# Performance work log

Measured on AMD Instinct MI355X. Metric: run time of the kernel, lower is better.

## Reference

```python
import jax, jax.numpy as jnp
from jax import lax
import numpy as np

EPS = 2.220446049250313e-16  # sys.float_info.epsilon


def setup_inputs() -> dict:
    key = jax.random.key(0)
    k1, k2, k3, k4 = jax.random.split(key, 4)
    C, H, W, R = 256, 256, 256, 16
    x = jax.random.normal(k1, (1, C, H, W), dtype=jnp.float32)
    w1 = jax.random.normal(k2, (R, C), dtype=jnp.float32) * 0.05   # Linear(C -> C//r), no bias
    w2 = jax.random.normal(k3, (C, R), dtype=jnp.float32) * 0.05   # Linear(C//r -> C), no bias
    conv_w = jax.random.normal(k4, (1, 2, 7, 7), dtype=jnp.float32) * 0.05  # Conv2d(2,1,7)
    return {"x": x, "w1": w1, "w2": w2, "conv_w": conv_w, "kv": 1}


def reference(x, w1, w2, conv_w, kv):
    b, c, h, w = x.shape  # b == 1 (module assumes batch 1 via squeeze(0))

    def fc(v):  # shared MLP of the channel attention
        return jnp.maximum(v @ w1.T, 0.0) @ w2.T

    y_avg = fc(x.mean(axis=(2, 3)))          # [1, C]
    y_max = fc(x.max(axis=(2, 3)))           # [1, C]
    y = jax.nn.sigmoid(y_avg + y_max)        # [1, C]

    yc = y[0]
    yc = (yc - yc.min()) / (yc.max() - yc.min() + 1e-20)  # min-max normalized gates in [0,1]

    # Batched SVD over channels replaces the per-channel Python loop.
    mats = x[0]                                            # [C, H, W]
    u, s, vh = jnp.linalg.svd(mats, full_matrices=False)   # u:[C,H,K] s:[C,K] vh:[C,K,W]
    K = s.shape[-1]
    # k = int(len(s) * kv * yc[c]); singular values are sorted descending, so
    # top-k selection == keep the first k -> mask the tail.
    k = jnp.floor(K * kv * yc).astype(jnp.int32)           # [C]
    keep = jnp.arange(K)[None, :] < k[:, None]             # [C, K]
    s_m = jnp.where(keep, s, 0.0)
    recon = jnp.einsum('chk,ck,ckw->chw', u, s_m, vh)      # low-rank reconstruction
    x2 = recon[None]                                       # [1, C, H, W]

    avg_out = x2.mean(axis=1, keepdims=True)
    max_out = x2.max(axis=1, keepdims=True)
    cat = jnp.concatenate([avg_out, max_out], axis=1)      # [1, 2, H, W]
    out = lax.conv_general_dilated(cat, conv_w, (1, 1), [(3, 3), (3, 3)],
                                   dimension_numbers=('NCHW', 'OIHW', 'NCHW'))
    out = jnp.where(out < EPS, EPS, out)
    return jax.nn.sigmoid(out)
```

## Files before the change

### kernel.cpp

```cpp
#include <hip/hip_runtime.h>


#define NCH 256
#define N 256
#define NN 65536
#define NS_MAX 22

#define OFF_K 0
#define OFF_MODE 256
#define OFF_MC 512
#define OFF_COEF 768
#define OFF_SUM 12032
#define OFF_MAXHW 77568
#define OFF_MEAND 143104
#define OFF_MAXD 143616
#define OFF_T 144128
#define OFF_ALPHA 144640
#define OFF_AQ 145152
#define OFF_BQ 276224
#define OFF_ITSW 407296
#define SMALL_FLOATS 407552

#define NSH_LDS 135168
#define F16_PANEL 33792

static const float EPSF = 2.220446049250313e-16f;

typedef unsigned short u16;
typedef _Float16 h8 __attribute__((ext_vector_type(8)));
typedef float f32x4 __attribute__((ext_vector_type(4)));

__device__ __forceinline__ float rdlane(float v, int l) {
  return __uint_as_float(__builtin_amdgcn_readlane(__float_as_uint(v), l));
}

__device__ __forceinline__ u16 f2h(float v) {
  _Float16 h = (_Float16)v;
  u16 u;
  __builtin_memcpy(&u, &h, 2);
  return u;
}
__device__ __forceinline__ float h2f(u16 u) {
  _Float16 h;
  __builtin_memcpy(&h, &u, 2);
  return (float)h;
}

__global__ __launch_bounds__(256) void k_chan_stats(const float* __restrict__ x,
                                                    float* __restrict__ small) {
  int c = blockIdx.x, tid = threadIdx.x;
  const float4* xc = (const float4*)(x + (size_t)c * NN);
  double s = 0.0;
  float m = -1e30f;
  for (int i = tid; i < NN / 4; i += 256) {
    float4 v = xc[i];
    s += (double)v.x + (double)v.y + (double)v.z + (double)v.w;
    m = fmaxf(m, fmaxf(fmaxf(v.x, v.y), fmaxf(v.z, v.w)));
  }
  __shared__ double rs[4];
  __shared__ float rm[4];
  for (int off = 32; off; off >>= 1) {
    s += __shfl_down(s, off, 64);
    m = fmaxf(m, __shfl_down(m, off, 64));
  }
  if ((tid & 63) == 0) { rs[tid >> 6] = s; rm[tid >> 6] = m; }
  __syncthreads();
  if (tid == 0) {
    ((double*)(small + OFF_MEAND))[c] = (rs[0] + rs[1] + rs[2] + rs[3]) / (double)NN;
    ((double*)(small + OFF_MAXD))[c] =
        (double)fmaxf(fmaxf(rm[0], rm[1]), fmaxf(rm[2], rm[3]));
  }
}

__global__ __launch_bounds__(256) void k_attention(const float* __restrict__ w1,
                                                   const float* __restrict__ w2,
                                                   const int* __restrict__ kvp,
                                                   float* __restrict__ small) {
  int tid = threadIdx.x;
  __shared__ double ha[16], hm[16], redd[8], ymn[256], ymx[256];
  double va = ((const double*)(small + OFF_MEAND))[tid];
  double vm = ((const double*)(small + OFF_MAXD))[tid];
  for (int r = 0; r < 16; ++r) {
    double wv = (double)w1[r * 256 + tid];
    double pa = wv * va, pm = wv * vm;
    for (int off = 32; off; off >>= 1) {
      pa += __shfl_down(pa, off, 64);
      pm += __shfl_down(pm, off, 64);
    }
    if ((tid & 63) == 0) { redd[tid >> 6] = pa; redd[4 + (tid >> 6)] = pm; }
    __syncthreads();
    if (tid == 0) {
      ha[r] = fmax(redd[0] + redd[1] + redd[2] + redd[3], 0.0);
      hm[r] = fmax(redd[4] + redd[5] + redd[6] + redd[7], 0.0);
    }
    __syncthreads();
  }
  double ya = 0.0, ym = 0.0;
  for (int r = 0; r < 16; ++r) {
    double wv = (double)w2[tid * 16 + r];
    ya += ha[r] * wv;
    ym += hm[r] * wv;
  }
  double y = 1.0 / (1.0 + exp(-(ya + ym)));
  ymn[tid] = y; ymx[tid] = y;
  __syncthreads();
  for (int off = 128; off; off >>= 1) {
    if (tid < off) {
      ymn[tid] = fmin(ymn[tid], ymn[tid + off]);
      ymx[tid] = fmax(ymx[tid], ymx[tid + off]);
    }
    __syncthreads();
  }
  double yc = (y - ymn[0]) / (ymx[0] - ymn[0] + 1e-20);
  int kv = kvp[0];
  int k = (int)floor(256.0 * (double)kv * yc);
  int mode = (k <= 0) ? 0 : ((k >= 256) ? 1 : 2);
  int* ip = (int*)small;
  ip[OFF_K + tid] = k;
  ip[OFF_MODE + tid] = mode;
}

#define GEMM128_VARS                                                           \
  int tid = threadIdx.x;                                                       \
  int tx4 = (tid & 15) * 4, ty4 = (tid >> 4) * 4;                              \
  int lm = tid >> 1, lq = (tid & 1) * 2;                                       \
  int lk = tid >> 4, lc = (tid & 15) * 2;                                      \
  (void)lk; (void)lc;

#define STORE_T128(Ls, v0, v1)                                                 \
  Ls[lq * 4 + 0][lm] = v0.x; Ls[lq * 4 + 1][lm] = v0.y;                        \
  Ls[lq * 4 + 2][lm] = v0.z; Ls[lq * 4 + 3][lm] = v0.w;                        \
  Ls[lq * 4 + 4][lm] = v1.x; Ls[lq * 4 + 5][lm] = v1.y;                        \
  Ls[lq * 4 + 6][lm] = v1.z; Ls[lq * 4 + 7][lm] = v1.w;

#define GEMM128_INNER(AsM, BsM)                                                \
  _Pragma("unroll") for (int kk = 0; kk < 16; ++kk) {                          \
    float4 a0 = *(const float4*)&AsM[kk][ty4];                                 \
    float4 a1 = *(const float4*)&AsM[kk][64 + ty4];                            \
    float4 b0 = *(const float4*)&BsM[kk][tx4];                                 \
    float4 b1 = *(const float4*)&BsM[kk][64 + tx4];                            \
    float av[8] = {a0.x, a0.y, a0.z, a0.w, a1.x, a1.y, a1.z, a1.w};            \
    float bv[8] = {b0.x, b0.y, b0.z, b0.w, b1.x, b1.y, b1.z, b1.w};            \
    _Pragma("unroll") for (int rr = 0; rr < 8; ++rr)                           \
      _Pragma("unroll") for (int cc2 = 0; cc2 < 8; ++cc2)                      \
        acc[rr][cc2] += av[rr] * bv[cc2];                                      \
  }

#define WRITE_TILE_NORM(Cc)                                                    \
  _Pragma("unroll") for (int rh = 0; rh < 2; ++rh)                             \
  _Pragma("unroll") for (int rr = 0; rr < 4; ++rr) {                           \
    int rI = rh * 4 + rr;                                                      \
    float* rowp = (Cc) + (size_t)(i0 + rh * 64 + ty4 + rr) * N + j0;           \
    *(float4*)(rowp + tx4) =                                                   \
        make_float4(acc[rI][0], acc[rI][1], acc[rI][2], acc[rI][3]);           \
    *(float4*)(rowp + 64 + tx4) =                                              \
        make_float4(acc[rI][4], acc[rI][5], acc[rI][6], acc[rI][7]);           \
  }

#define WRITE_TILE_MIRROR(Cc)                                                  \
  _Pragma("unroll") for (int ch = 0; ch < 2; ++ch)                             \
  _Pragma("unroll") for (int cc2 = 0; cc2 < 4; ++cc2) {                        \
    int cI = ch * 4 + cc2;                                                     \
    float* rowp = (Cc) + (size_t)(j0 + ch * 64 + tx4 + cc2) * N + i0;          \
    *(float4*)(rowp + ty4) =                                                   \
        make_float4(acc[0][cI], acc[1][cI], acc[2][cI], acc[3][cI]);           \
    *(float4*)(rowp + 64 + ty4) =                                              \
        make_float4(acc[4][cI], acc[5][cI], acc[6][cI], acc[7][cI]);           \
  }

#define SYM_MAP                                                                \
  int bx = blockIdx.x;                                                         \
  int i0 = (bx >= 1) ? 128 : 0, j0 = (bx == 2) ? 128 : 0;

__global__ __launch_bounds__(256) void k_gram(const float* __restrict__ x,
                                              float* __restrict__ bufA, int base) {
  __shared__ float As[16][132], Bs[16][132];
  GEMM128_VARS; SYM_MAP;
  const float* A = x + (size_t)(base + blockIdx.z) * NN;
  float acc[8][8] = {};
  const float* Ap = A + (size_t)(i0 + lm) * N + lq * 4;
  const float* Bp = A + (size_t)(j0 + lm) * N + lq * 4;
  float4 va0 = *(const float4*)Ap, va1 = *(const float4*)(Ap + 4);
  float4 vb0 = *(const float4*)Bp, vb1 = *(const float4*)(Bp + 4);
  for (int kt = 0; kt < 16; ++kt) {
    __syncthreads();
    STORE_T128(As, va0, va1); STORE_T128(Bs, vb0, vb1);
    __syncthreads();
    if (kt < 15) {
      va0 = *(const float4*)(Ap + (kt + 1) * 16);
      va1 = *(const float4*)(Ap + (kt + 1) * 16 + 4);
      vb0 = *(const float4*)(Bp + (kt + 1) * 16);
      vb1 = *(const float4*)(Bp + (kt + 1) * 16 + 4);
    }
    GEMM128_INNER(As, Bs);
  }
  float* Cc = bufA + (size_t)blockIdx.z * NN;
  WRITE_TILE_NORM(Cc);
  if (bx == 1) { WRITE_TILE_MIRROR(Cc); }
}

__device__ __forceinline__ double mv_chunk(const float* __restrict__ P, int c0,
                                           int j, int r, int R0, int triR,
                                           float ureg) {
  double pi0 = 0.0, pi1 = 0.0, pi2 = 0.0, pi3 = 0.0;
  if (c0 < N) {
    int lbeg = (c0 > j + 1) ? c0 : (j + 1);
    int lend = c0 + 64;
    if (lbeg < lend) {
      if (c0 + 64 <= R0) {
        int lmv = lbeg;
        for (; lmv + 3 < lend; lmv += 4) {
          float uv0 = rdlane(ureg, lmv - c0), uv1 = rdlane(ureg, lmv + 1 - c0);
          float uv2 = rdlane(ureg, lmv + 2 - c0), uv3 = rdlane(ureg, lmv + 3 - c0);
          float v0 = P[triR + lmv], v1 = P[triR + lmv + 1];
          float v2 = P[triR + lmv + 2], v3 = P[triR + lmv + 3];
          pi0 += (double)v0 * (double)uv0;
          pi1 += (double)v1 * (double)uv1;
          pi2 += (double)v2 * (double)uv2;
          pi3 += (double)v3 * (double)uv3;
        }
        for (; lmv < lend; ++lmv)
          pi0 += (double)P[triR + lmv] * (double)rdlane(ureg, lmv - c0);
      } else if (c0 >= R0 + 64) {
        int lmv = lbeg;
        int s = (lmv * (lmv + 1)) >> 1;
        for (; lmv + 3 < lend; lmv += 4) {
          int s0 = s, s1 = s0 + lmv + 1, s2 = s1 + lmv + 2, s3 = s2 + lmv + 3;
          s = s3 + lmv + 4;
          float uv0 = rdlane(ureg, lmv - c0), uv1 = rdlane(ureg, lmv + 1 - c0);
          float uv2 = rdlane(ureg, lmv + 2 - c0), uv3 = rdlane(ureg, lmv + 3 - c0);
          pi0 += (double)P[s0 + r] * (double)uv0;
          pi1 += (double)P[s1 + r] * (double)uv1;
          pi2 += (double)P[s2 + r] * (double)uv2;
          pi3 += (double)P[s3 + r] * (double)uv3;
        }
        for (; lmv < lend; ++lmv) {
          pi0 += (double)P[s + r] * (double)rdlane(ureg, lmv - c0);
          s += lmv + 1;
        }
      } else {
        int lmv = lbeg;
        int s = (lmv * (lmv + 1)) >> 1;
        for (; lmv < lend; ++lmv) {
          float uv = rdlane(ureg, lmv - c0);
          float v = P[(lmv <= r) ? (triR + lmv) : (s + r)];
          pi0 += (double)v * (double)uv;
          s += lmv + 1;
        }
      }
    }
  }
  return (pi0 + pi1) + (pi2 + pi3);
}

__device__ __forceinline__ void upd_chunk(float* __restrict__ P, int c0, int j,
                                          int r, int R0, int triR, float ureg,
                                          float wreg, float urf, float wrf) {
  if (c0 >= N) return;
  int lbeg = (c0 > j + 1) ? c0 : (j + 1);
  int lend = c0 + 64;
  int lcap = (r | 63) + 1;
  if (lend > lcap) lend = lcap;
  if (c0 + 64 <= R0) {
    int lmv = lbeg;
    for (; lmv + 1 < lend; lmv += 2) {
      float uv0 = rdlane(ureg, lmv - c0), wv0 = rdlane(wreg, lmv - c0);
      float uv1 = rdlane(ureg, lmv + 1 - c0), wv1 = rdlane(wreg, lmv + 1 - c0);
      P[triR + lmv] = fmaf(-wrf, uv0, fmaf(-urf, wv0, P[triR + lmv]));
      P[triR + lmv + 1] = fmaf(-wrf, uv1, fmaf(-urf, wv1, P[triR + lmv + 1]));
    }
    if (lmv < lend) {
      float uv0 = rdlane(ureg, lmv - c0), wv0 = rdlane(wreg, lmv - c0);
      P[triR + lmv] = fmaf(-wrf, uv0, fmaf(-urf, wv0, P[triR + lmv]));
    }
  } else if (c0 == R0) {
    for (int lmv = lbeg; lmv < lend; ++lmv) {
      float uv = rdlane(ureg, lmv - c0), wv = rdlane(wreg, lmv - c0);
      if (lmv <= r)
        P[triR + lmv] = fmaf(-wrf, uv, fmaf(-urf, wv, P[triR + lmv]));
    }
  }
}

__global__ __launch_bounds__(1024) void k_tridiag(const float* __restrict__ Gall,
                                                  float* __restrict__ small, int base) {
  extern __shared__ double dls[];
  double* redd = dls;
  double* redd2 = dls + 16;
  double* pip = dls + 32;
  float* P = (float*)(dls + 1056);
  float* uf = P + 32896;
  float* wf = uf + 256;
  int tid = threadIdx.x, lane = tid & 63;
  int r = tid & 255, g = tid >> 8;
  int wid = tid >> 6;
  int R0 = (wid & 3) << 6;
  int c = base + blockIdx.x;
  const int* ip = (const int*)small;
  if (ip[OFF_MODE + c] != 2) return;
  const float* G = Gall + (size_t)blockIdx.x * NN;
  double* aq = (double*)(small + OFF_AQ) + (size_t)c * 256;
  double* bq = (double*)(small + OFF_BQ) + (size_t)c * 256;
  const int triR = (r * (r + 1)) >> 1;

  for (int i = g; i < N; i += 4)
    if (r <= i) P[((i * (i + 1)) >> 1) + r] = G[i * N + r];
  __syncthreads();

  for (int j = 0; j + 2 < N; ++j) {
    if (g == 0 && r >= j + 1) uf[r] = P[triR + j];
    __syncthreads();
    float x_r = uf[r];
    double x0 = (double)uf[j + 1];
    int cbase = (j + 1) & ~63;
    int c0 = cbase + 64 * g;
    float ureg = 0.f;
    if (c0 < N) ureg = uf[c0 + lane];
    double sp = (g == 0 && r >= j + 2) ? (double)x_r * (double)x_r : 0.0;
    double myp = mv_chunk(P, c0, j, r, R0, triR, ureg);
    pip[tid] = (r >= j + 1) ? myp : 0.0;
    for (int off = 32; off; off >>= 1) sp += __shfl_down(sp, off, 64);
    if (lane == 0) redd[wid] = sp;
    __syncthreads();
    double sigma = (((redd[0] + redd[1]) + (redd[2] + redd[3])) +
                    ((redd[4] + redd[5]) + (redd[6] + redd[7]))) +
                   (((redd[8] + redd[9]) + (redd[10] + redd[11])) +
                    ((redd[12] + redd[13]) + (redd[14] + redd[15])));
    if (sigma <= 1e-40) {
      if (tid == 0) bq[j] = x0;
      continue;
    }
    double nu = sqrt(x0 * x0 + sigma);
    double bsub = (x0 >= 0.0) ? -nu : nu;
    double beta = 1.0 / (nu * (nu + fabs(x0)));
    if (c0 <= j + 1 && j + 1 < c0 + 64 && lane == j + 1 - c0)
      ureg = (float)(x0 - bsub);
    double pi = 0.0, u_r = 0.0, kp = 0.0;
    if (r >= j + 1) {
      double fix = -bsub * (double)P[triR + (j + 1)];
      pi = (pip[r] + pip[256 + r] + pip[512 + r] + pip[768 + r] + fix) * beta;
      u_r = (r == j + 1) ? (x0 - bsub) : (double)x_r;
      kp = u_r * pi * 0.25;
    }
    for (int off = 32; off; off >>= 1) kp += __shfl_down(kp, off, 64);
    if (lane == 0) redd2[wid] = kp;
    __syncthreads();
    double K = ((((redd2[0] + redd2[1]) + (redd2[2] + redd2[3])) +
                 ((redd2[4] + redd2[5]) + (redd2[6] + redd2[7]))) +
                (((redd2[8] + redd2[9]) + (redd2[10] + redd2[11])) +
                 ((redd2[12] + redd2[13]) + (redd2[14] + redd2[15])))) *
               beta * 0.5;
    if (g == 0 && r >= j + 1) wf[r] = (float)(pi - K * u_r);
    __syncthreads();
    float wreg = 0.f;
    if (c0 < N) wreg = wf[c0 + lane];
    if (r >= j + 1) {
      float urf = (float)u_r;
      float wrf = wf[r];
      upd_chunk(P, c0, j, r, R0, triR, ureg, wreg, urf, wrf);
    }
    if (tid == 0) bq[j] = bsub;
    __syncthreads();
  }
  if (g == 0) aq[r] = (double)P[triR + r];
  if (tid == 0) bq[N - 2] = (double)P[(((N - 1) * N) >> 1) + N - 2];
}

__device__ __forceinline__ int sturm_count_lds(const double* a, const double* b,
                                               double t) {
  double d = a[0] - t;
  int cnt = (d < 0.0);
  for (int i = 1; i < N; ++i) {
    double den = d;
    if (fabs(den) < 1e-20) den = (den < 0.0) ? -1e-20 : 1e-20;
    double bb = b[i - 1];
    d = (a[i] - t) - bb * bb / den;
    cnt += (d < 0.0);
  }
  return cnt;
}

__global__ __launch_bounds__(64) void k_bisect(float* __restrict__ small,
                                               int base, int cc) {
  int ci = blockIdx.x;
  if (ci >= cc) return;
  int c = base + ci, lane = threadIdx.x;
  int* ip = (int*)small;
  if (ip[OFF_MODE + c] != 2) {
    if (lane == 0) { ip[OFF_MC + c] = 0; ip[OFF_ITSW + c] = 0; }
    return;
  }
  int k = ip[OFF_K + c];
  const double* a = (const double*)(small + OFF_AQ) + (size_t)c * 256;
  const double* b = (const double*)(small + OFF_BQ) + (size_t)c * 256;
  __shared__ double sa[256], sb[256];
  for (int i = lane; i < N; i += 64) {
    sa[i] = a[i];
    if (i < N - 1) sb[i] = b[i];
  }
  __syncthreads();
  double lo = 1e300, hi = -1e300;
  for (int i = lane; i < N; i += 64) {
    double rr = (i > 0 ? fabs(sb[i - 1]) : 0.0) + (i < N - 1 ? fabs(sb[i]) : 0.0);
    lo = fmin(lo, sa[i] - rr);
    hi = fmax(hi, sa[i] + rr);
  }
  for (int off = 32; off; off >>= 1) {
    lo = fmin(lo, __shfl_xor(lo, off, 64));
    hi = fmax(hi, __shfl_xor(hi, off, 64));
  }
  double lamk = 0.0, lamk1 = 0.0;
  for (int which = 0; which < 2; ++which) {
    int j = (which == 0) ? (N - k + 1) : (N - k);
    double l0 = lo, h0 = hi;
    for (int pass = 0; pass < 10; ++pass) {
      double step = (h0 - l0) * (1.0 / 65.0);
      double t = l0 + step * (double)(lane + 1);
      int cnt = sturm_count_lds(sa, sb, t);
      unsigned long long mask = __ballot(cnt >= j);
      if (mask == 0ull) {
        l0 = l0 + step * 64.0;
      } else {
        int bpos = __ffsll((long long)mask) - 1;
        double nl = (bpos == 0) ? l0 : (l0 + step * (double)bpos);
        h0 = l0 + step * (double)(bpos + 1);
        l0 = nl;
      }
    }
    double v = 0.5 * (l0 + h0);
    if (which == 0) lamk = v; else lamk1 = v;
  }
  if (lane == 0) {
    double t = 0.5 * (lamk + lamk1);
    double gap = fmax(lamk - lamk1, 0.0);
    double alpha = 1.002 * fmax(hi - t, t - lo) + 1e-30;
    double g0 = fmax(gap / (2.0 * alpha), 2e-6);
    float* cf = small + OFF_COEF + (size_t)c * (2 * NS_MAX);
    double l = fmin(g0, 0.99);
    int m = 0, isw = NS_MAX;
    while (m < NS_MAX - 2 && l < 0.9999) {
      if (isw == NS_MAX && l >= 0.02) isw = m;
      double aa = sqrt(27.0 / (4.0 * (1.0 + l + l * l)));
      double bb = (4.0 / 27.0) * aa * aa * aa;
      cf[2 * m] = (float)aa;
      cf[2 * m + 1] = (float)bb;
      double pl = aa * l - bb * l * l * l;
      double p1 = aa - bb;
      l = fmin(pl, p1);
      m++;
    }
    for (int e = 0; e < 2; ++e) {
      if (isw == NS_MAX && l >= 0.02) isw = m;
      cf[2 * m] = 1.5f; cf[2 * m + 1] = 0.5f; m++;
    }
    if (isw > m) isw = m;
    ip[OFF_MC + c] = m;
    ip[OFF_ITSW + c] = isw;
    ((double*)(small + OFF_T))[c] = t;
    ((double*)(small + OFF_ALPHA))[c] = alpha;
  }
}

__global__ void k_x0(const float* __restrict__ small, float* __restrict__ bufA,
                     int base) {
  int ci = blockIdx.y, c = base + ci;
  const int* ip = (const int*)small;
  if (ip[OFF_MODE + c] != 2) return;
  double t = ((const double*)(small + OFF_T))[c];
  double inva = 1.0 / ((const double*)(small + OFF_ALPHA))[c];
  float* X = bufA + (size_t)ci * NN;
  int r = blockIdx.x, tid = threadIdx.x;
  double gg = (double)X[r * N + tid];
  if (tid == r) gg -= t;
  X[r * N + tid] = (float)(gg * inva);
}

__global__ __launch_bounds__(256) void k_ns1(const float* __restrict__ src,
                                             float* __restrict__ Sb,
                                             const float* __restrict__ small,
                                             int base, int it) {
  const int* ip = (const int*)small;
  int c = base + blockIdx.z;
  if (ip[OFF_MODE + c] != 2 || it >= ip[OFF_ITSW + c]) return;
  __shared__ float As[16][132], Bs[16][132];
  GEMM128_VARS; SYM_MAP;
  const float* X = src + (size_t)blockIdx.z * NN;
  float acc[8][8] = {};
  const float* Ap = X + (size_t)(i0 + lm) * N + lq * 4;
  const float* Bp = X + (size_t)(j0 + lm) * N + lq * 4;
  float4 va0 = *(const float4*)Ap, va1 = *(const float4*)(Ap + 4);
  float4 vb0 = *(const float4*)Bp, vb1 = *(const float4*)(Bp + 4);
  for (int kt = 0; kt < 16; ++kt) {
    __syncthreads();
    STORE_T128(As, va0, va1); STORE_T128(Bs, vb0, vb1);
    __syncthreads();
    if (kt < 15) {
      va0 = *(const float4*)(Ap + (kt + 1) * 16);
      va1 = *(const float4*)(Ap + (kt + 1) * 16 + 4);
      vb0 = *(const float4*)(Bp + (kt + 1) * 16);
      vb1 = *(const float4*)(Bp + (kt + 1) * 16 + 4);
    }
    GEMM128_INNER(As, Bs);
  }
  float* Cc = Sb + (size_t)blockIdx.z * NN;
  WRITE_TILE_NORM(Cc);
  if (bx == 1) { WRITE_TILE_MIRROR(Cc); }
}

__global__ __launch_bounds__(256) void k_ns2(const float* __restrict__ src,
                                             const float* __restrict__ Sb,
                                             float* __restrict__ dst,
                                             const float* __restrict__ small,
                                             int base, int it) {
  const int* ip = (const int*)small;
  int c = base + blockIdx.z;
  if (ip[OFF_MODE + c] != 2 || it >= ip[OFF_ITSW + c]) return;
  float ca = small[OFF_COEF + (size_t)c * (2 * NS_MAX) + 2 * it];
  float cb = small[OFF_COEF + (size_t)c * (2 * NS_MAX) + 2 * it + 1];
  __shared__ float As[16][132], Bs[16][132];
  GEMM128_VARS; SYM_MAP;
  const float* X = src + (size_t)blockIdx.z * NN;
  const float* S = Sb + (size_t)blockIdx.z * NN;
  float acc[8][8] = {};
  const float* Ap = X + (size_t)(i0 + lm) * N + lq * 4;
  const float* Bp = S + (size_t)(j0 + lm) * N + lq * 4;
  float4 va0 = *(const float4*)Ap, va1 = *(const float4*)(Ap + 4);
  float4 vb0 = *(const float4*)Bp, vb1 = *(const float4*)(Bp + 4);
  for (int kt = 0; kt < 16; ++kt) {
    __syncthreads();
    STORE_T128(As, va0, va1); STORE_T128(Bs, vb0, vb1);
    __syncthreads();
    if (kt < 15) {
      va0 = *(const float4*)(Ap + (kt + 1) * 16);
      va1 = *(const float4*)(Ap + (kt + 1) * 16 + 4);
      vb0 = *(const float4*)(Bp + (kt + 1) * 16);
      vb1 = *(const float4*)(Bp + (kt + 1) * 16 + 4);
    }
    GEMM128_INNER(As, Bs);
  }
#pragma unroll
  for (int rh = 0; rh < 2; ++rh)
#pragma unroll
    for (int rr = 0; rr < 4; ++rr) {
      int rI = rh * 4 + rr;
      const float* rowp = X + (size_t)(i0 + rh * 64 + ty4 + rr) * N + j0;
      float4 x0 = *(const float4*)(rowp + tx4);
      float4 x1 = *(const float4*)(rowp + 64 + tx4);
      acc[rI][0] = ca * x0.x - cb * acc[rI][0];
      acc[rI][1] = ca * x0.y - cb * acc[rI][1];
      acc[rI][2] = ca * x0.z - cb * acc[rI][2];
      acc[rI][3] = ca * x0.w - cb * acc[rI][3];
      acc[rI][4] = ca * x1.x - cb * acc[rI][4];
      acc[rI][5] = ca * x1.y - cb * acc[rI][5];
      acc[rI][6] = ca * x1.z - cb * acc[rI][6];
      acc[rI][7] = ca * x1.w - cb * acc[rI][7];
    }
  float* Y = dst + (size_t)blockIdx.z * NN;
  WRITE_TILE_NORM(Y);
  if (bx == 1) { WRITE_TILE_MIRROR(Y); }
}

__device__ __forceinline__ void stage_h(u16* pan, const u16* g16, int tid) {
#pragma unroll
  for (int i = 0; i < 16; ++i) {
    int g = tid * 16 + i * 4096;
    int lo = g + ((g >> 9) << 4);
    *(uint4*)((char*)pan + lo) = *(const uint4*)((const char*)g16 + g);
  }
}
__device__ __forceinline__ void stage_f(u16* pan, const float* gF, int tid) {
#pragma unroll
  for (int i = 0; i < 16; ++i) {
    int e = tid * 8 + i * 2048;
    float4 v0 = *(const float4*)(gF + e);
    float4 v1 = *(const float4*)(gF + e + 4);
    h8 hv;
    hv[0] = (_Float16)v0.x; hv[1] = (_Float16)v0.y;
    hv[2] = (_Float16)v0.z; hv[3] = (_Float16)v0.w;
    hv[4] = (_Float16)v1.x; hv[5] = (_Float16)v1.y;
    hv[6] = (_Float16)v1.z; hv[7] = (_Float16)v1.w;
    int b = e * 2;
    int lo = b + ((b >> 9) << 4);
    *(h8*)((char*)pan + lo) = hv;
  }
}

__global__ __launch_bounds__(256) void k_nsh(const float* __restrict__ srcF,
                                             float* __restrict__ Sf,
                                             float* __restrict__ dstF,
                                             const float* __restrict__ small,
                                             int base, int it, int phase) {
  const int* ip = (const int*)small;
  int ci = blockIdx.z, c = base + ci;
  if (ip[OFF_MODE + c] != 2) return;
  int isw = ip[OFF_ITSW + c], mc = ip[OFF_MC + c];
  if (it < isw || it >= mc) return;
  SYM_MAP;
  extern __shared__ char ldsraw[];
  u16* Apan = (u16*)ldsraw;
  u16* Bpan = Apan + F16_PANEL;
  int tid = threadIdx.x;
  bool cvtA = (it == isw);
  bool sameP = (phase == 0) && (bx != 1);
  const float* XF = srcF + (size_t)ci * NN;
  const u16* XH = (const u16*)XF;
  if (cvtA) stage_f(Apan, XF + (size_t)i0 * N, tid);
  else      stage_h(Apan, XH + (size_t)i0 * N, tid);
  if (!sameP) {
    if (phase == 0) {
      if (cvtA) stage_f(Bpan, XF + (size_t)j0 * N, tid);
      else      stage_h(Bpan, XH + (size_t)j0 * N, tid);
    } else {
      const u16* SH = (const u16*)(Sf + (size_t)ci * NN);
      stage_h(Bpan, SH + (size_t)j0 * N, tid);
    }
  }
  const u16* Bb = sameP ? Apan : Bpan;
  __syncthreads();

  int l = tid & 63, wid = tid >> 6;
  int wr = (wid >> 1) * 64, wc = (wid & 1) * 64;
  int rA = wr + (l & 15), rB = wc + (l & 15);
  int kB = (l >> 4) << 3;
  f32x4 zero = {0.f, 0.f, 0.f, 0.f};
  f32x4 acc[4][4];
#pragma unroll
  for (int mi = 0; mi < 4; ++mi)
#pragma unroll
    for (int ni = 0; ni < 4; ++ni) acc[mi][ni] = zero;

#pragma unroll
  for (int kc = 0; kc < 8; ++kc) {
    int kof = kc * 32 + kB;
    h8 af[4], bf[4];
#pragma unroll
    for (int mi = 0; mi < 4; ++mi)
      af[mi] = *(const h8*)((const char*)Apan +
                            ((size_t)(rA + mi * 16) * 264 + kof) * 2);
#pragma unroll
    for (int ni = 0; ni < 4; ++ni)
      bf[ni] = *(const h8*)((const char*)Bb +
                            ((size_t)(rB + ni * 16) * 264 + kof) * 2);
#pragma unroll
    for (int mi = 0; mi < 4; ++mi)
#pragma unroll
      for (int ni = 0; ni < 4; ++ni)
        acc[mi][ni] = __builtin_amdgcn_mfma_f32_16x16x32_f16(
            af[mi], bf[ni], acc[mi][ni], 0, 0, 0);
  }

  float cav = 0.f, cbv = 0.f;
  bool last = false;
  if (phase) {
    cav = small[OFF_COEF + (size_t)c * (2 * NS_MAX) + 2 * it];
    cbv = small[OFF_COEF + (size_t)c * (2 * NS_MAX) + 2 * it + 1];
    last = (it == mc - 1);
  }
  float* oF = dstF + (size_t)ci * NN;
  u16* oH = phase ? (u16*)oF : (u16*)(Sf + (size_t)ci * NN);
  int lr4 = (l >> 4) << 2, lcn = l & 15;
#pragma unroll
  for (int mi = 0; mi < 4; ++mi)
#pragma unroll
    for (int ni = 0; ni < 4; ++ni)
#pragma unroll
      for (int rg = 0; rg < 4; ++rg) {
        int gr = i0 + wr + mi * 16 + lr4 + rg;
        int gc = j0 + wc + ni * 16 + lcn;
        float v = acc[mi][ni][rg];
        if (phase) {
          float xv = h2f(Apan[(size_t)(gr - i0) * 264 + gc]);
          v = cav * xv - cbv * v;
        }
        if (!last) {
          u16 hv = f2h(v);
          oH[(size_t)gr * N + gc] = hv;
          if (bx == 1) oH[(size_t)gc * N + gr] = hv;
        } else {
          oF[(size_t)gr * N + gc] = v;
          if (bx == 1) oF[(size_t)gc * N + gr] = v;
        }
      }
}

__global__ __launch_bounds__(256) void k_proj(const float* __restrict__ bufA,
                                              const float* __restrict__ bufB,
                                              const float* __restrict__ x,
                                              float* __restrict__ bufC,
                                              const float* __restrict__ small,
                                              int base) {
  const int* ip = (const int*)small;
  int ci = blockIdx.z, c = base + ci;
  int mode = ip[OFF_MODE + c];
  GEMM128_VARS;
  int i0 = blockIdx.x * 128, j0 = blockIdx.y * 128;
  float* Cc = bufC + (size_t)ci * NN;
  const float* xc = x + (size_t)c * NN;
  if (mode != 2) {
#pragma unroll
    for (int rh = 0; rh < 2; ++rh)
#pragma unroll
      for (int rr = 0; rr < 4; ++rr) {
        size_t ro = (size_t)(i0 + rh * 64 + ty4 + rr) * N + j0;
        if (mode == 0) {
          *(float4*)(Cc + ro + tx4) = make_float4(0.f, 0.f, 0.f, 0.f);
          *(float4*)(Cc + ro + 64 + tx4) = make_float4(0.f, 0.f, 0.f, 0.f);
        } else {
          *(float4*)(Cc + ro + tx4) = *(const float4*)(xc + ro + tx4);
          *(float4*)(Cc + ro + 64 + tx4) = *(const float4*)(xc + ro + 64 + tx4);
        }
      }
    return;
  }
  int mc = ip[OFF_MC + c];
  const float* Xh = ((mc & 1) ? bufB : bufA) + (size_t)ci * NN;
  __shared__ float As[16][132], Bs[16][132];
  float acc[8][8] = {};
  const float* Ap = Xh + (size_t)(i0 + lm) * N + lq * 4;
  const float* Bp = xc + (size_t)lk * N + j0 + lc * 4;
  float4 va0 = *(const float4*)Ap, va1 = *(const float4*)(Ap + 4);
  float4 vb0 = *(const float4*)Bp, vb1 = *(const float4*)(Bp + 4);
  for (int kt = 0; kt < 16; ++kt) {
    __syncthreads();
    STORE_T128(As, va0, va1);
    *(float4*)&Bs[lk][lc * 4] = vb0;
    *(float4*)&Bs[lk][(lc + 1) * 4] = vb1;
    __syncthreads();
    if (kt < 15) {
      va0 = *(const float4*)(Ap + (kt + 1) * 16);
      va1 = *(const float4*)(Ap + (kt + 1) * 16 + 4);
      const float* Bp2 = xc + (size_t)((kt + 1) * 16 + lk) * N + j0 + lc * 4;
      vb0 = *(const float4*)Bp2;
      vb1 = *(const float4*)(Bp2 + 4);
    }
    GEMM128_INNER(As, Bs);
  }
#pragma unroll
  for (int rh = 0; rh < 2; ++rh)
#pragma unroll
    for (int rr = 0; rr < 4; ++rr) {
      int rI = rh * 4 + rr;
      const float* rowp = xc + (size_t)(i0 + rh * 64 + ty4 + rr) * N + j0;
      float4 x0 = *(const float4*)(rowp + tx4);
      float4 x1 = *(const float4*)(rowp + 64 + tx4);
      acc[rI][0] = 0.5f * (acc[rI][0] + x0.x);
      acc[rI][1] = 0.5f * (acc[rI][1] + x0.y);
      acc[rI][2] = 0.5f * (acc[rI][2] + x0.z);
      acc[rI][3] = 0.5f * (acc[rI][3] + x0.w);
      acc[rI][4] = 0.5f * (acc[rI][4] + x1.x);
      acc[rI][5] = 0.5f * (acc[rI][5] + x1.y);
      acc[rI][6] = 0.5f * (acc[rI][6] + x1.z);
      acc[rI][7] = 0.5f * (acc[rI][7] + x1.w);
    }
  WRITE_TILE_NORM(Cc);
}

__global__ void k_accum(const float* __restrict__ bufC, float* __restrict__ sum_hw,
                        float* __restrict__ max_hw, int cc, int first) {
  int p = blockIdx.x * 256 + threadIdx.x;
  float s = first ? 0.f : sum_hw[p];
  float m = first ? -1e30f : max_hw[p];
  for (int ci = 0; ci < cc; ++ci) {
    float v = bufC[(size_t)ci * NN + p];
    s += v;
    m = fmaxf(m, v);
  }
  sum_hw[p] = s;
  max_hw[p] = m;
}

__global__ void k_conv(const float* __restrict__ sum_hw, const float* __restrict__ max_hw,
                       const float* __restrict__ cw, float* __restrict__ out) {
  int p = blockIdx.x * 256 + threadIdx.x;
  int h = p >> 8, w = p & 255;
  float acc = 0.f;
  for (int dy = 0; dy < 7; ++dy) {
    int hy = h + dy - 3;
    if (hy < 0 || hy > 255) continue;
    for (int dx = 0; dx < 7; ++dx) {
      int wx = w + dx - 3;
      if (wx < 0 || wx > 255) continue;
      int q = hy * 256 + wx;
      acc += cw[dy * 7 + dx] * (sum_hw[q] * (1.f / 256.f)) +
             cw[49 + dy * 7 + dx] * max_hw[q];
    }
  }
  acc = fmaxf(acc, EPSF);
  out[p] = 1.f / (1.f + expf(-acc));
}

extern "C" void kernel_launch(void* const* d_in, const int* in_sizes, int n_in,
                              void* d_out, int out_size, void* d_ws, size_t ws_size,
                              hipStream_t stream) {
  const float* x = (const float*)d_in[0];
  const float* w1 = (const float*)d_in[1];
  const float* w2 = (const float*)d_in[2];
  const float* cw = (const float*)d_in[3];
  const int* kv = (const int*)d_in[4];
  float* out = (float*)d_out;
  float* small = (float*)d_ws;

  size_t small_bytes = (size_t)SMALL_FLOATS * 4;
  size_t avail = ws_size > small_bytes ? ws_size - small_bytes : 0;
  long chunk = (long)(avail / (3ull * NN * 4));
  if (chunk > NCH) chunk = NCH;
  if (chunk < 1) chunk = 1;
  float* bufA = small + SMALL_FLOATS;
  float* bufB = bufA + (size_t)chunk * NN;
  float* bufC = bufB + (size_t)chunk * NN;

  const int tridiag_lds = 1056 * 8 + 32896 * 4 + 512 * 4;
  hipFuncSetAttribute((const void*)k_tridiag,
                      hipFuncAttributeMaxDynamicSharedMemorySize, tridiag_lds);
  hipFuncSetAttribute((const void*)k_nsh,
                      hipFuncAttributeMaxDynamicSharedMemorySize, NSH_LDS);

  k_chan_stats<<<NCH, 256, 0, stream>>>(x, small);
  k_attention<<<1, 256, 0, stream>>>(w1, w2, kv, small);

  const int IT32 = 13;

  for (int base = 0; base < NCH; base += (int)chunk) {
    int cc = (NCH - base < (int)chunk) ? (NCH - base) : (int)chunk;
    dim3 gsym(3, 1, cc);
    dim3 gproj(2, 2, cc);
    k_gram<<<gsym, 256, 0, stream>>>(x, bufA, base);
    k_tridiag<<<cc, 1024, tridiag_lds, stream>>>(bufA, small, base);
    k_bisect<<<cc, 64, 0, stream>>>(small, base, cc);
    k_x0<<<dim3(N, cc), 256, 0, stream>>>(small, bufA, base);
    for (int it = 0; it < NS_MAX; ++it) {
      const float* src = (it & 1) ? bufB : bufA;
      float* dst = (it & 1) ? bufA : bufB;
      if (it < IT32) {
        k_ns1<<<gsym, 256, 0, stream>>>(src, bufC, small, base, it);
        k_ns2<<<gsym, 256, 0, stream>>>(src, bufC, dst, small, base, it);
      }
      k_nsh<<<gsym, 256, NSH_LDS, stream>>>(src, bufC, dst, small, base, it, 0);
      k_nsh<<<gsym, 256, NSH_LDS, stream>>>(src, bufC, dst, small, base, it, 1);
    }
    k_proj<<<gproj, 256, 0, stream>>>(bufA, bufB, x, bufC, small, base);
    k_accum<<<256, 256, 0, stream>>>(bufC, small + OFF_SUM, small + OFF_MAXHW, cc,
                                     base == 0 ? 1 : 0);
  }
  k_conv<<<256, 256, 0, stream>>>(small + OFF_SUM, small + OFF_MAXHW, cw, out);
}
```

Measured before the change: 5.601 ms.

## Fuse both Newton-Schulz half-steps into one per-channel kernel with LDS-resident matrix

The two k_nsh launches per iteration (square, then combine) are replaced by a single k_nsf kernel. It launches one 512-thread block per channel and stages the whole fp16 256x256 matrix in LDS once. The first product is written to global scratch in fp16 with mirroring for the symmetric off-diagonal block. After a threadfence and block barrier, the same block reads it back for the second product and the final combine. This halves kernel launches and removes the repeated panel staging across three tiles per channel. In exchange, the second GEMM's B operand comes from global/L2 instead of LDS, two of the eight waves sit idle on the skipped upper block, and there are fewer, larger blocks per launch.

```diff
diff --git a/kernel.cpp b/kernel.cpp
--- a/kernel.cpp
+++ b/kernel.cpp
@@ -21,8 +21,7 @@
 #define OFF_ITSW 407296
 #define SMALL_FLOATS 407552
 
-#define NSH_LDS 135168
-#define F16_PANEL 33792
+#define NSF_LDS 135168
 
 static const float EPSF = 2.220446049250313e-16f;
 
@@ -560,127 +559,139 @@
   if (bx == 1) { WRITE_TILE_MIRROR(Y); }
 }
 
-__device__ __forceinline__ void stage_h(u16* pan, const u16* g16, int tid) {
-#pragma unroll
-  for (int i = 0; i < 16; ++i) {
-    int g = tid * 16 + i * 4096;
-    int lo = g + ((g >> 9) << 4);
-    *(uint4*)((char*)pan + lo) = *(const uint4*)((const char*)g16 + g);
-  }
-}
-__device__ __forceinline__ void stage_f(u16* pan, const float* gF, int tid) {
-#pragma unroll
-  for (int i = 0; i < 16; ++i) {
-    int e = tid * 8 + i * 2048;
-    float4 v0 = *(const float4*)(gF + e);
-    float4 v1 = *(const float4*)(gF + e + 4);
-    h8 hv;
-    hv[0] = (_Float16)v0.x; hv[1] = (_Float16)v0.y;
-    hv[2] = (_Float16)v0.z; hv[3] = (_Float16)v0.w;
-    hv[4] = (_Float16)v1.x; hv[5] = (_Float16)v1.y;
-    hv[6] = (_Float16)v1.z; hv[7] = (_Float16)v1.w;
-    int b = e * 2;
-    int lo = b + ((b >> 9) << 4);
-    *(h8*)((char*)pan + lo) = hv;
-  }
-}
-
-__global__ __launch_bounds__(256) void k_nsh(const float* __restrict__ srcF,
+__global__ __launch_bounds__(512) void k_nsf(const float* __restrict__ srcF,
                                              float* __restrict__ Sf,
                                              float* __restrict__ dstF,
                                              const float* __restrict__ small,
-                                             int base, int it, int phase) {
+                                             int base, int it) {
   const int* ip = (const int*)small;
-  int ci = blockIdx.z, c = base + ci;
+  int ci = blockIdx.x, c = base + ci;
   if (ip[OFF_MODE + c] != 2) return;
   int isw = ip[OFF_ITSW + c], mc = ip[OFF_MC + c];
   if (it < isw || it >= mc) return;
-  SYM_MAP;
   extern __shared__ char ldsraw[];
-  u16* Apan = (u16*)ldsraw;
-  u16* Bpan = Apan + F16_PANEL;
+  u16* Xl = (u16*)ldsraw;
   int tid = threadIdx.x;
-  bool cvtA = (it == isw);
-  bool sameP = (phase == 0) && (bx != 1);
   const float* XF = srcF + (size_t)ci * NN;
   const u16* XH = (const u16*)XF;
-  if (cvtA) stage_f(Apan, XF + (size_t)i0 * N, tid);
-  else      stage_h(Apan, XH + (size_t)i0 * N, tid);
-  if (!sameP) {
-    if (phase == 0) {
-      if (cvtA) stage_f(Bpan, XF + (size_t)j0 * N, tid);
-      else      stage_h(Bpan, XH + (size_t)j0 * N, tid);
-    } else {
-      const u16* SH = (const u16*)(Sf + (size_t)ci * NN);
-      stage_h(Bpan, SH + (size_t)j0 * N, tid);
-    }
-  }
-  const u16* Bb = sameP ? Apan : Bpan;
+  if (it == isw) {
+#pragma unroll
+    for (int i = 0; i < 16; ++i) {
+      int e = tid * 8 + i * 4096;
+      float4 v0 = *(const float4*)(XF + e);
+      float4 v1 = *(const float4*)(XF + e + 4);
+      h8 hv;
+      hv[0] = (_Float16)v0.x; hv[1] = (_Float16)v0.y;
+      hv[2] = (_Float16)v0.z; hv[3] = (_Float16)v0.w;
+      hv[4] = (_Float16)v1.x; hv[5] = (_Float16)v1.y;
+      hv[6] = (_Float16)v1.z; hv[7] = (_Float16)v1.w;
+      *(h8*)&Xl[(e >> 8) * 264 + (e & 255)] = hv;
+    }
+  } else {
+#pragma unroll
+    for (int i = 0; i < 16; ++i) {
+      int e = tid * 8 + i * 4096;
+      *(uint4*)&Xl[(e >> 8) * 264 + (e & 255)] = *(const uint4*)(XH + e);
+    }
+  }
   __syncthreads();
 
   int l = tid & 63, wid = tid >> 6;
-  int wr = (wid >> 1) * 64, wc = (wid & 1) * 64;
-  int rA = wr + (l & 15), rB = wc + (l & 15);
-  int kB = (l >> 4) << 3;
+  int r0 = (wid >> 1) * 64, cB = (wid & 1) * 128;
+  int rl = l & 15, kB = (l >> 4) << 3, lr4 = (l >> 4) << 2;
+  int rb = r0 >> 7, cb2 = cB >> 7;
+  bool diagw = (rb == cb2);
+  bool mirw = (rb > cb2);
+  bool skipw = (rb < cb2);
+  u16* SH = (u16*)(Sf + (size_t)ci * NN);
   f32x4 zero = {0.f, 0.f, 0.f, 0.f};
-  f32x4 acc[4][4];
-#pragma unroll
-  for (int mi = 0; mi < 4; ++mi)
-#pragma unroll
-    for (int ni = 0; ni < 4; ++ni) acc[mi][ni] = zero;
-
-#pragma unroll
-  for (int kc = 0; kc < 8; ++kc) {
-    int kof = kc * 32 + kB;
-    h8 af[4], bf[4];
+  f32x4 acc[4][8];
+
+  if (!skipw) {
 #pragma unroll
     for (int mi = 0; mi < 4; ++mi)
-      af[mi] = *(const h8*)((const char*)Apan +
-                            ((size_t)(rA + mi * 16) * 264 + kof) * 2);
-#pragma unroll
-    for (int ni = 0; ni < 4; ++ni)
-      bf[ni] = *(const h8*)((const char*)Bb +
-                            ((size_t)(rB + ni * 16) * 264 + kof) * 2);
+#pragma unroll
+      for (int ni = 0; ni < 8; ++ni) acc[mi][ni] = zero;
+#pragma unroll
+    for (int kc = 0; kc < 8; ++kc) {
+      int kof = kc * 32 + kB;
+      h8 af[4], bf[8];
+#pragma unroll
+      for (int mi = 0; mi < 4; ++mi)
+        af[mi] = *(const h8*)&Xl[(size_t)(r0 + mi * 16 + rl) * 264 + kof];
+#pragma unroll
+      for (int ni = 0; ni < 8; ++ni)
+        bf[ni] = *(const h8*)&Xl[(size_t)(cB + ni * 16 + rl) * 264 + kof];
+#pragma unroll
+      for (int mi = 0; mi < 4; ++mi)
+#pragma unroll
+        for (int ni = 0; ni < 8; ++ni)
+          acc[mi][ni] = __builtin_amdgcn_mfma_f32_16x16x32_f16(
+              af[mi], bf[ni], acc[mi][ni], 0, 0, 0);
+    }
 #pragma unroll
     for (int mi = 0; mi < 4; ++mi)
 #pragma unroll
-      for (int ni = 0; ni < 4; ++ni)
-        acc[mi][ni] = __builtin_amdgcn_mfma_f32_16x16x32_f16(
-            af[mi], bf[ni], acc[mi][ni], 0, 0, 0);
-  }
-
-  float cav = 0.f, cbv = 0.f;
-  bool last = false;
-  if (phase) {
-    cav = small[OFF_COEF + (size_t)c * (2 * NS_MAX) + 2 * it];
-    cbv = small[OFF_COEF + (size_t)c * (2 * NS_MAX) + 2 * it + 1];
-    last = (it == mc - 1);
-  }
-  float* oF = dstF + (size_t)ci * NN;
-  u16* oH = phase ? (u16*)oF : (u16*)(Sf + (size_t)ci * NN);
-  int lr4 = (l >> 4) << 2, lcn = l & 15;
-#pragma unroll
-  for (int mi = 0; mi < 4; ++mi)
-#pragma unroll
-    for (int ni = 0; ni < 4; ++ni)
-#pragma unroll
-      for (int rg = 0; rg < 4; ++rg) {
-        int gr = i0 + wr + mi * 16 + lr4 + rg;
-        int gc = j0 + wc + ni * 16 + lcn;
-        float v = acc[mi][ni][rg];
-        if (phase) {
-          float xv = h2f(Apan[(size_t)(gr - i0) * 264 + gc]);
-          v = cav * xv - cbv * v;
+      for (int ni = 0; ni < 8; ++ni)
+#pragma unroll
+        for (int rg = 0; rg < 4; ++rg) {
+          int gr = r0 + mi * 16 + lr4 + rg;
+          int gc = cB + ni * 16 + rl;
+          u16 hv = f2h(acc[mi][ni][rg]);
+          SH[(size_t)gr * N + gc] = hv;
+          if (mirw) SH[(size_t)gc * N + gr] = hv;
         }
-        if (!last) {
-          u16 hv = f2h(v);
-          oH[(size_t)gr * N + gc] = hv;
-          if (bx == 1) oH[(size_t)gc * N + gr] = hv;
-        } else {
-          oF[(size_t)gr * N + gc] = v;
-          if (bx == 1) oF[(size_t)gc * N + gr] = v;
+  }
+  __threadfence();
+  __syncthreads();
+
+  float cav = small[OFF_COEF + (size_t)c * (2 * NS_MAX) + 2 * it];
+  float cbv = small[OFF_COEF + (size_t)c * (2 * NS_MAX) + 2 * it + 1];
+  bool last = (it == mc - 1);
+  if (!skipw) {
+#pragma unroll
+    for (int mi = 0; mi < 4; ++mi)
+#pragma unroll
+      for (int ni = 0; ni < 8; ++ni) acc[mi][ni] = zero;
+#pragma unroll
+    for (int kc = 0; kc < 8; ++kc) {
+      int kof = kc * 32 + kB;
+      h8 af[4], bf[8];
+#pragma unroll
+      for (int mi = 0; mi < 4; ++mi)
+        af[mi] = *(const h8*)&Xl[(size_t)(r0 + mi * 16 + rl) * 264 + kof];
+#pragma unroll
+      for (int ni = 0; ni < 8; ++ni)
+        bf[ni] = *(const h8*)(SH + (size_t)(cB + ni * 16 + rl) * N + kof);
+#pragma unroll
+      for (int mi = 0; mi < 4; ++mi)
+#pragma unroll
+        for (int ni = 0; ni < 8; ++ni)
+          acc[mi][ni] = __builtin_amdgcn_mfma_f32_16x16x32_f16(
+              af[mi], bf[ni], acc[mi][ni], 0, 0, 0);
+    }
+    float* oF = dstF + (size_t)ci * NN;
+    u16* oH = (u16*)oF;
+#pragma unroll
+    for (int mi = 0; mi < 4; ++mi)
+#pragma unroll
+      for (int ni = 0; ni < 8; ++ni)
+#pragma unroll
+        for (int rg = 0; rg < 4; ++rg) {
+          int gr = r0 + mi * 16 + lr4 + rg;
+          int gc = cB + ni * 16 + rl;
+          float xv = h2f(Xl[(size_t)gr * 264 + gc]);
+          float v = cav * xv - cbv * acc[mi][ni][rg];
+          if (!last) {
+            u16 hv = f2h(v);
+            oH[(size_t)gr * N + gc] = hv;
+            if (mirw) oH[(size_t)gc * N + gr] = hv;
+          } else {
+            oF[(size_t)gr * N + gc] = v;
+            if (mirw) oF[(size_t)gc * N + gr] = v;
+          }
         }
-      }
+  }
 }
 
 __global__ __launch_bounds__(256) void k_proj(const float* __restrict__ bufA,
@@ -812,8 +823,8 @@
   const int tridiag_lds = 1056 * 8 + 32896 * 4 + 512 * 4;
   hipFuncSetAttribute((const void*)k_tridiag,
                       hipFuncAttributeMaxDynamicSharedMemorySize, tridiag_lds);
-  hipFuncSetAttribute((const void*)k_nsh,
-                      hipFuncAttributeMaxDynamicSharedMemorySize, NSH_LDS);
+  hipFuncSetAttribute((const void*)k_nsf,
+                      hipFuncAttributeMaxDynamicSharedMemorySize, NSF_LDS);
 
   k_chan_stats<<<NCH, 256, 0, stream>>>(x, small);
   k_attention<<<1, 256, 0, stream>>>(w1, w2, kv, small);
@@ -835,8 +846,7 @@
         k_ns1<<<gsym, 256, 0, stream>>>(src, bufC, small, base, it);
         k_ns2<<<gsym, 256, 0, stream>>>(src, bufC, dst, small, base, it);
       }
-      k_nsh<<<gsym, 256, NSH_LDS, stream>>>(src, bufC, dst, small, base, it, 0);
-      k_nsh<<<gsym, 256, NSH_LDS, stream>>>(src, bufC, dst, small, base, it, 1);
+      k_nsf<<<cc, 512, NSF_LDS, stream>>>(src, bufC, dst, small, base, it);
     }
     k_proj<<<gproj, 256, 0, stream>>>(bufA, bufB, x, bufC, small, base);
     k_accum<<<256, 256, 0, stream>>>(bufC, small + OFF_SUM, small + OFF_MAXHW, cc,
```

Measured after the change: 5.796 ms. 3.5% more time.
